# Optimization experiments

Hardware: AMD Instinct MI355X
Metric: run time of the kernel (lower is better)

The kernel has to match this reference:

```python
import jax, jax.numpy as jnp
import numpy as np
from jax import lax

B, T, I, H, O = 2048, 2048, 1, 64, 1


def setup_inputs() -> dict:
    key = jax.random.key(0)
    ks = jax.random.split(key, 7)
    s_ih = 1.0 / np.sqrt(H)  # PyTorch nn.RNN/Linear init scale (uniform(-1/sqrt(H), 1/sqrt(H)))
    return {
        "x": jax.random.normal(ks[0], (B, T, I), dtype=jnp.float32),
        "W_ih": jax.random.uniform(ks[1], (H, I), jnp.float32, -s_ih, s_ih),
        "W_hh": jax.random.uniform(ks[2], (H, H), jnp.float32, -s_ih, s_ih),
        "b_ih": jax.random.uniform(ks[3], (H,), jnp.float32, -s_ih, s_ih),
        "b_hh": jax.random.uniform(ks[4], (H,), jnp.float32, -s_ih, s_ih),
        "W_fc": jax.random.uniform(ks[5], (O, H), jnp.float32, -s_ih, s_ih),
        "b_fc": jax.random.uniform(ks[6], (O,), jnp.float32, -s_ih, s_ih),
    }


def reference(x, W_ih, W_hh, b_ih, b_hh, W_fc, b_fc):
    # Precompute the input projection for all timesteps in one GEMM:
    # pre[b,t,h] = x @ W_ih^T + b_ih + b_hh   (biases folded in once)
    pre = jnp.einsum('bti,hi->bth', x, W_ih) + (b_ih + b_hh)  # [B,T,H]
    pre_t = jnp.swapaxes(pre, 0, 1)  # [T,B,H] for scan over time

    def step(h, xt):
        # h_t = tanh(W_ih x_t + b_ih + W_hh h_{t-1} + b_hh)
        h_new = jnp.tanh(xt + h @ W_hh.T)
        return h_new, None

    h0 = jnp.zeros((x.shape[0], W_hh.shape[0]), dtype=x.dtype)
    h_last, _ = lax.scan(step, h0, pre_t)
    # Linear head on the last hidden state: out[:, -1, :] -> fc
    return h_last @ W_fc.T + b_fc  # [B, O]
```

## Files before the change

### kernel.cpp

```cpp
#include <hip/hip_runtime.h>

#define B_ 2048
#define T_ 2048
#define SPW 16
#define GSTR 162
#define QT 512
#define XSTR 516

typedef _Float16 f16x8 __attribute__((ext_vector_type(8)));
typedef float    f32x4 __attribute__((ext_vector_type(4)));
typedef unsigned u32x2 __attribute__((ext_vector_type(2)));
typedef unsigned u32x4 __attribute__((ext_vector_type(4)));

__device__ __forceinline__ unsigned pkrtz(float lo, float hi) {
    return __builtin_bit_cast(unsigned, __builtin_amdgcn_cvt_pkrtz(lo, hi));
}

__global__ __launch_bounds__(256)
void rnn_mfma_4w3(
    const float* __restrict__ x, const float* __restrict__ W_ih,
    const float* __restrict__ W_hh, const float* __restrict__ b_ih,
    const float* __restrict__ b_hh, const float* __restrict__ W_fc,
    const float* __restrict__ b_fc, float* __restrict__ out)
{
    __shared__ __align__(16) float xl[SPW * XSTR];
    __shared__ __align__(16) unsigned ex[2][4 * GSTR];
    __shared__ float fcb[4][SPW];

    const int tid = threadIdx.x;
    const int w = tid >> 6;
    const int l = tid & 63;
    const int s = l & 15;
    const int g = l >> 4;
    const int sb = blockIdx.x * SPW;
    const float L2E2 = 2.8853900817779268f;

    f16x8 a0, a1;
#pragma unroll
    for (int j = 0; j < 8; ++j) {
        const int k0 = 16 * (0 + (j >> 2)) + 4 * g + (j & 3);
        const int k1 = 16 * (2 + (j >> 2)) + 4 * g + (j & 3);
        a0[j] = (_Float16)(W_hh[(16 * w + s) * 64 + k0] * L2E2);
        a1[j] = (_Float16)(W_hh[(16 * w + s) * 64 + k1] * L2E2);
    }

    float wih[4], bw[4];
#pragma unroll
    for (int r = 0; r < 4; ++r) {
        const int row = 16 * w + 4 * g + r;
        wih[r] = W_ih[row] * L2E2;
        bw[r]  = (b_ih[row] + b_hh[row]) * L2E2;
    }

    const int exbase = g * GSTR + s * 10;
    unsigned* const wr0 = &ex[0][exbase + 2 * w];
    unsigned* const wr1 = &ex[1][exbase + 2 * w];
    const unsigned* const rd0 = &ex[0][exbase];
    const unsigned* const rd1 = &ex[1][exbase];

    float h[4] = {0.0f, 0.0f, 0.0f, 0.0f};

    const float* xg = x + (size_t)sb * T_;
    const float* const xrow = &xl[s * XSTR];

    for (int q = 0; q < 4; ++q) {
        __syncthreads();
#pragma unroll
        for (int i = 0; i < 2; ++i) {
            const int it  = tid + 256 * i;
        }
        for (int it = tid; it < SPW * (QT / 4); it += 256) {
            const int row = it >> 7;
            const int c4  = it & 127;
            const float4 v =
                *(const float4*)(xg + (size_t)row * T_ + q * QT + 4 * c4);
            *(float4*)&xl[row * XSTR + 4 * c4] = v;
        }
        __syncthreads();

        for (int t0 = 0; t0 < QT; t0 += 4) {
            const float4 xq = *(const float4*)(xrow + t0);
            const float xa[4] = {xq.x, xq.y, xq.z, xq.w};

#pragma unroll
            for (int j4 = 0; j4 < 4; ++j4) {
                const int buf = j4 & 1;

                const u32x2 pk = {pkrtz(h[0], h[1]), pkrtz(h[2], h[3])};
                *(u32x2*)(buf ? wr1 : wr0) = pk;
                __syncthreads();

                const unsigned* rp = buf ? rd1 : rd0;
                const u32x2 e0 = *(const u32x2*)(rp + 0);
                const u32x2 e1 = *(const u32x2*)(rp + 2);
                const u32x2 e2 = *(const u32x2*)(rp + 4);
                const u32x2 e3 = *(const u32x2*)(rp + 6);
                const u32x4 q0 = {e0.x, e0.y, e1.x, e1.y};
                const u32x4 q1 = {e2.x, e2.y, e3.x, e3.y};
                const f16x8 b0 = __builtin_bit_cast(f16x8, q0);
                const f16x8 b1 = __builtin_bit_cast(f16x8, q1);

                f32x4 ci;
#pragma unroll
                for (int r = 0; r < 4; ++r) ci[r] = fmaf(xa[j4], wih[r], bw[r]);
                const f32x4 p0 =
                    __builtin_amdgcn_mfma_f32_16x16x32_f16(a0, b0, ci, 0, 0, 0);
                const f32x4 acc =
                    __builtin_amdgcn_mfma_f32_16x16x32_f16(a1, b1, p0, 0, 0, 0);

#pragma unroll
                for (int r = 0; r < 4; ++r) {
                    const float e = __builtin_amdgcn_exp2f(acc[r]);
                    h[r] = fmaf(-2.0f, __builtin_amdgcn_rcpf(e + 1.0f), 1.0f);
                }
            }
        }
    }

    float p = 0.0f;
#pragma unroll
    for (int r = 0; r < 4; ++r) p = fmaf(h[r], W_fc[16 * w + 4 * g + r], p);
    p += __shfl_down(p, 32);
    p += __shfl_down(p, 16);
    if (l < 16) fcb[w][l] = p;
    __syncthreads();
    if (tid < 16)
        out[sb + tid] = (fcb[0][tid] + fcb[1][tid]) + (fcb[2][tid] + fcb[3][tid]) + b_fc[0];
}

extern "C" void kernel_launch(void* const* d_in, const int* in_sizes, int n_in,
                              void* d_out, int out_size, void* d_ws, size_t ws_size,
                              hipStream_t stream) {
    const float* x    = (const float*)d_in[0];
    const float* W_ih = (const float*)d_in[1];
    const float* W_hh = (const float*)d_in[2];
    const float* b_ih = (const float*)d_in[3];
    const float* b_hh = (const float*)d_in[4];
    const float* W_fc = (const float*)d_in[5];
    const float* b_fc = (const float*)d_in[6];
    float* out = (float*)d_out;

    rnn_mfma_4w3<<<dim3(B_ / SPW), dim3(256), 0, stream>>>(x, W_ih, W_hh, b_ih, b_hh,
                                                           W_fc, b_fc, out);
}
```

Baseline: 343.0 us.

## Interleave two independent sequence groups per block to hide step latency

Each block now handles 32 sequences as two independent 16-sequence groups whose recurrence steps are interleaved, sharing one barrier per step. The x staging tile is halved in time length to keep LDS usage similar. This is meant to hide the serial MFMA/transcendental/LDS latency chain using instruction-level parallelism. In exchange, half as many blocks are launched, so fewer CUs are used, and register pressure per thread rises.

```diff
diff --git a/kernel.cpp b/kernel.cpp
--- a/kernel.cpp
+++ b/kernel.cpp
@@ -2,10 +2,10 @@
 
 #define B_ 2048
 #define T_ 2048
-#define SPW 16
+#define SPB 32
 #define GSTR 162
-#define QT 512
-#define XSTR 516
+#define QT 256
+#define XSTR 260
 
 typedef _Float16 f16x8 __attribute__((ext_vector_type(8)));
 typedef float    f32x4 __attribute__((ext_vector_type(4)));
@@ -17,22 +17,22 @@
 }
 
 __global__ __launch_bounds__(256)
-void rnn_mfma_4w3(
+void rnn_mfma_2g(
     const float* __restrict__ x, const float* __restrict__ W_ih,
     const float* __restrict__ W_hh, const float* __restrict__ b_ih,
     const float* __restrict__ b_hh, const float* __restrict__ W_fc,
     const float* __restrict__ b_fc, float* __restrict__ out)
 {
-    __shared__ __align__(16) float xl[SPW * XSTR];
-    __shared__ __align__(16) unsigned ex[2][4 * GSTR];
-    __shared__ float fcb[4][SPW];
+    __shared__ __align__(16) float xl[SPB * XSTR];
+    __shared__ __align__(16) unsigned ex[2][2][4 * GSTR];
+    __shared__ float fcb[4][SPB];
 
     const int tid = threadIdx.x;
     const int w = tid >> 6;
     const int l = tid & 63;
     const int s = l & 15;
     const int g = l >> 4;
-    const int sb = blockIdx.x * SPW;
+    const int sb = blockIdx.x * SPB;
     const float L2E2 = 2.8853900817779268f;
 
     f16x8 a0, a1;
@@ -53,25 +53,23 @@
     }
 
     const int exbase = g * GSTR + s * 10;
-    unsigned* const wr0 = &ex[0][exbase + 2 * w];
-    unsigned* const wr1 = &ex[1][exbase + 2 * w];
-    const unsigned* const rd0 = &ex[0][exbase];
-    const unsigned* const rd1 = &ex[1][exbase];
+    unsigned* const wrA[2] = {&ex[0][0][exbase + 2 * w], &ex[0][1][exbase + 2 * w]};
+    unsigned* const wrB[2] = {&ex[1][0][exbase + 2 * w], &ex[1][1][exbase + 2 * w]};
+    const unsigned* const rdA[2] = {&ex[0][0][exbase], &ex[0][1][exbase]};
+    const unsigned* const rdB[2] = {&ex[1][0][exbase], &ex[1][1][exbase]};
 
-    float h[4] = {0.0f, 0.0f, 0.0f, 0.0f};
+    float hA[4] = {0.f, 0.f, 0.f, 0.f};
+    float hB[4] = {0.f, 0.f, 0.f, 0.f};
 
     const float* xg = x + (size_t)sb * T_;
-    const float* const xrow = &xl[s * XSTR];
+    const float* const xrowA = &xl[s * XSTR];
+    const float* const xrowB = &xl[(16 + s) * XSTR];
 
-    for (int q = 0; q < 4; ++q) {
+    for (int q = 0; q < T_ / QT; ++q) {
         __syncthreads();
-#pragma unroll
-        for (int i = 0; i < 2; ++i) {
-            const int it  = tid + 256 * i;
-        }
-        for (int it = tid; it < SPW * (QT / 4); it += 256) {
-            const int row = it >> 7;
-            const int c4  = it & 127;
+        for (int it = tid; it < SPB * (QT / 4); it += 256) {
+            const int row = it >> 6;
+            const int c4  = it & 63;
             const float4 v =
                 *(const float4*)(xg + (size_t)row * T_ + q * QT + 4 * c4);
             *(float4*)&xl[row * XSTR + 4 * c4] = v;
@@ -79,53 +77,85 @@
         __syncthreads();
 
         for (int t0 = 0; t0 < QT; t0 += 4) {
-            const float4 xq = *(const float4*)(xrow + t0);
-            const float xa[4] = {xq.x, xq.y, xq.z, xq.w};
+            const float4 xqA = *(const float4*)(xrowA + t0);
+            const float4 xqB = *(const float4*)(xrowB + t0);
+            const float xaA[4] = {xqA.x, xqA.y, xqA.z, xqA.w};
+            const float xaB[4] = {xqB.x, xqB.y, xqB.z, xqB.w};
 
 #pragma unroll
             for (int j4 = 0; j4 < 4; ++j4) {
                 const int buf = j4 & 1;
 
-                const u32x2 pk = {pkrtz(h[0], h[1]), pkrtz(h[2], h[3])};
-                *(u32x2*)(buf ? wr1 : wr0) = pk;
+                const u32x2 pkA = {pkrtz(hA[0], hA[1]), pkrtz(hA[2], hA[3])};
+                *(u32x2*)wrA[buf] = pkA;
+                const u32x2 pkB = {pkrtz(hB[0], hB[1]), pkrtz(hB[2], hB[3])};
+                *(u32x2*)wrB[buf] = pkB;
+
                 __syncthreads();
 
-                const unsigned* rp = buf ? rd1 : rd0;
-                const u32x2 e0 = *(const u32x2*)(rp + 0);
-                const u32x2 e1 = *(const u32x2*)(rp + 2);
-                const u32x2 e2 = *(const u32x2*)(rp + 4);
-                const u32x2 e3 = *(const u32x2*)(rp + 6);
-                const u32x4 q0 = {e0.x, e0.y, e1.x, e1.y};
-                const u32x4 q1 = {e2.x, e2.y, e3.x, e3.y};
-                const f16x8 b0 = __builtin_bit_cast(f16x8, q0);
-                const f16x8 b1 = __builtin_bit_cast(f16x8, q1);
+                const unsigned* rpA = rdA[buf];
+                const u32x2 eA0 = *(const u32x2*)(rpA + 0);
+                const u32x2 eA1 = *(const u32x2*)(rpA + 2);
+                const u32x2 eA2 = *(const u32x2*)(rpA + 4);
+                const u32x2 eA3 = *(const u32x2*)(rpA + 6);
+                const unsigned* rpB = rdB[buf];
+                const u32x2 eB0 = *(const u32x2*)(rpB + 0);
+                const u32x2 eB1 = *(const u32x2*)(rpB + 2);
+                const u32x2 eB2 = *(const u32x2*)(rpB + 4);
+                const u32x2 eB3 = *(const u32x2*)(rpB + 6);
+                const u32x4 qA0 = {eA0.x, eA0.y, eA1.x, eA1.y};
+                const u32x4 qA1 = {eA2.x, eA2.y, eA3.x, eA3.y};
+                const u32x4 qB0 = {eB0.x, eB0.y, eB1.x, eB1.y};
+                const u32x4 qB1 = {eB2.x, eB2.y, eB3.x, eB3.y};
+                const f16x8 bA0 = __builtin_bit_cast(f16x8, qA0);
+                const f16x8 bA1 = __builtin_bit_cast(f16x8, qA1);
+                const f16x8 bB0 = __builtin_bit_cast(f16x8, qB0);
+                const f16x8 bB1 = __builtin_bit_cast(f16x8, qB1);
 
-                f32x4 ci;
+                f32x4 ciA;
 #pragma unroll
-                for (int r = 0; r < 4; ++r) ci[r] = fmaf(xa[j4], wih[r], bw[r]);
-                const f32x4 p0 =
-                    __builtin_amdgcn_mfma_f32_16x16x32_f16(a0, b0, ci, 0, 0, 0);
-                const f32x4 acc =
-                    __builtin_amdgcn_mfma_f32_16x16x32_f16(a1, b1, p0, 0, 0, 0);
+                for (int r = 0; r < 4; ++r) ciA[r] = fmaf(xaA[j4], wih[r], bw[r]);
+                const f32x4 pA0 =
+                    __builtin_amdgcn_mfma_f32_16x16x32_f16(a0, bA0, ciA, 0, 0, 0);
+                const f32x4 accA =
+                    __builtin_amdgcn_mfma_f32_16x16x32_f16(a1, bA1, pA0, 0, 0, 0);
+
+                f32x4 ciB;
+#pragma unroll
+                for (int r = 0; r < 4; ++r) ciB[r] = fmaf(xaB[j4], wih[r], bw[r]);
+                const f32x4 pB0 =
+                    __builtin_amdgcn_mfma_f32_16x16x32_f16(a0, bB0, ciB, 0, 0, 0);
+                const f32x4 accB =
+                    __builtin_amdgcn_mfma_f32_16x16x32_f16(a1, bB1, pB0, 0, 0, 0);
 
 #pragma unroll
                 for (int r = 0; r < 4; ++r) {
-                    const float e = __builtin_amdgcn_exp2f(acc[r]);
-                    h[r] = fmaf(-2.0f, __builtin_amdgcn_rcpf(e + 1.0f), 1.0f);
+                    const float eA = __builtin_amdgcn_exp2f(accA[r]);
+                    hA[r] = fmaf(-2.0f, __builtin_amdgcn_rcpf(eA + 1.0f), 1.0f);
+                }
+#pragma unroll
+                for (int r = 0; r < 4; ++r) {
+                    const float eB = __builtin_amdgcn_exp2f(accB[r]);
+                    hB[r] = fmaf(-2.0f, __builtin_amdgcn_rcpf(eB + 1.0f), 1.0f);
                 }
             }
         }
     }
 
-    float p = 0.0f;
+    float pA = 0.0f, pB = 0.0f;
 #pragma unroll
-    for (int r = 0; r < 4; ++r) p = fmaf(h[r], W_fc[16 * w + 4 * g + r], p);
-    p += __shfl_down(p, 32);
-    p += __shfl_down(p, 16);
-    if (l < 16) fcb[w][l] = p;
+    for (int r = 0; r < 4; ++r) {
+        const float wf = W_fc[16 * w + 4 * g + r];
+        pA = fmaf(hA[r], wf, pA);
+        pB = fmaf(hB[r], wf, pB);
+    }
+    pA += __shfl_down(pA, 32); pA += __shfl_down(pA, 16);
+    pB += __shfl_down(pB, 32); pB += __shfl_down(pB, 16);
+    if (l < 16) { fcb[w][l] = pA; fcb[w][16 + l] = pB; }
     __syncthreads();
-    if (tid < 16)
-        out[sb + tid] = (fcb[0][tid] + fcb[1][tid]) + (fcb[2][tid] + fcb[3][tid]) + b_fc[0];
+    if (tid < SPB)
+        out[sb + tid] =
+            (fcb[0][tid] + fcb[1][tid]) + (fcb[2][tid] + fcb[3][tid]) + b_fc[0];
 }
 
 extern "C" void kernel_launch(void* const* d_in, const int* in_sizes, int n_in,
@@ -140,6 +170,6 @@
     const float* b_fc = (const float*)d_in[6];
     float* out = (float*)d_out;
 
-    rnn_mfma_4w3<<<dim3(B_ / SPW), dim3(256), 0, stream>>>(x, W_ih, W_hh, b_ih, b_hh,
-                                                           W_fc, b_fc, out);
+    rnn_mfma_2g<<<dim3(B_ / SPB), dim3(256), 0, stream>>>(x, W_ih, W_hh, b_ih, b_hh,
+                                                          W_fc, b_fc, out);
 }
```

Measured after the change: 545.0 us. +58.9%, slower.
